# Kernel tuning notes

Hardware: AMD Instinct MI355X
Metric: run time of the kernel (lower is better)

Reference implementation:

```python
import jax, jax.numpy as jnp
import numpy as np

B, N, U = 4, 4096, 512


def setup_inputs() -> dict:
    key = jax.random.key(0)
    ks = jax.random.split(key, 5)
    s = 1.0 / np.sqrt(U)
    return {
        "x": jax.random.normal(ks[0], (B, N, U), dtype=jnp.float32),
        "Wq": jax.random.normal(ks[1], (U, U), dtype=jnp.float32) * s,
        "bq": jnp.zeros((U,), dtype=jnp.float32),
        "Wk": jax.random.normal(ks[2], (U, U), dtype=jnp.float32) * s,
        "bk": jnp.zeros((U,), dtype=jnp.float32),
        "Wv": jax.random.normal(ks[3], (U, U), dtype=jnp.float32) * s,
        "bv": jnp.zeros((U,), dtype=jnp.float32),
        "Wp": jax.random.normal(ks[4], (U, U), dtype=jnp.float32) * s,
        "bp": jnp.zeros((U,), dtype=jnp.float32),
    }


def reference(x, Wq, bq, Wk, bk, Wv, bv, Wp, bp):
    # x: [B, N, U] single-head self-attention with residual
    scale = jnp.asarray(x.shape[-1], jnp.float32) ** -0.5
    q = x @ Wq + bq
    k = x @ Wk + bk
    v = x @ Wv + bv
    scores = jnp.einsum("bnd,bmd->bnm", q, k) * scale  # [B, N, N]
    attn = jax.nn.softmax(scores, axis=-1)
    ctx = jnp.einsum("bnm,bmd->bnd", attn, v)
    return x + (ctx @ Wp + bp)
```

## Files before the change

kernel.cpp:

```cpp
#include <hip/hip_runtime.h>
#include <hip/hip_bf16.h>
#include <math.h>

#define NB 4
#define NN 4096
#define UU 512

using short8   = __attribute__((ext_vector_type(8))) short;
using bf16x8   = __attribute__((ext_vector_type(8))) __bf16;
using floatx4  = __attribute__((ext_vector_type(4))) float;
using floatx16 = __attribute__((ext_vector_type(16))) float;

__device__ __forceinline__ floatx4 mfma16(short8 a, short8 b, floatx4 c) {
    return __builtin_amdgcn_mfma_f32_16x16x32_bf16(
        __builtin_bit_cast(bf16x8, a), __builtin_bit_cast(bf16x8, b), c, 0, 0, 0);
}
__device__ __forceinline__ floatx16 mfma32(short8 a, short8 b, floatx16 c) {
    return __builtin_amdgcn_mfma_f32_32x32x16_bf16(
        __builtin_bit_cast(bf16x8, a), __builtin_bit_cast(bf16x8, b), c, 0, 0, 0);
}

__device__ __forceinline__ unsigned short f2bf(float f) {
    union { float f; unsigned u; } v; v.f = f;
    return (unsigned short)((v.u + 0x7fffu + ((v.u >> 16) & 1u)) >> 16);
}
__device__ __forceinline__ float bf2f(unsigned short s) {
    union { unsigned u; float f; } v; v.u = ((unsigned)s) << 16; return v.f;
}

#define GLL16(gp, lp) __builtin_amdgcn_global_load_lds( \
    (const __attribute__((address_space(1))) void*)(gp), \
    (__attribute__((address_space(3))) void*)(lp), 16, 0, 0)

__global__ void __launch_bounds__(256) k_cvt_x(const float* __restrict__ x,
                                               unsigned short* __restrict__ xb) {
    int i = (blockIdx.x * 256 + threadIdx.x) * 4;
    float4 v = *(const float4*)(x + i);
    ushort4 o;
    o.x = f2bf(v.x); o.y = f2bf(v.y); o.z = f2bf(v.z); o.w = f2bf(v.w);
    *(ushort4*)(xb + i) = o;
}

__global__ void __launch_bounds__(256) k_cvt_w4(
    const float* __restrict__ Wq, const float* __restrict__ Wk,
    const float* __restrict__ Wv, const float* __restrict__ Wp,
    unsigned short* __restrict__ WTbase) {
    const int z = blockIdx.y;
    const float* W = (z == 0) ? Wq : (z == 1) ? Wk : (z == 2) ? Wv : Wp;
    int idx = blockIdx.x * 256 + threadIdx.x;
    int n = idx >> 9, k = idx & 511;
    WTbase[(size_t)z * 262144 + idx] = f2bf(W[k * 512 + n]);
}

__global__ void __launch_bounds__(256, 2) k_proj(
    const unsigned short* __restrict__ Xb,
    const unsigned short* __restrict__ WqT, const unsigned short* __restrict__ WkT,
    const unsigned short* __restrict__ WvT,
    const float* __restrict__ bq, const float* __restrict__ bk, const float* __restrict__ bv,
    unsigned short* __restrict__ Q, unsigned short* __restrict__ K8,
    unsigned short* __restrict__ V8)
{
    __shared__ __align__(16) unsigned short As[128 * 32];
    __shared__ __align__(16) unsigned short Bs[128 * 32];
    const int z = blockIdx.z;
    const unsigned short* WT = (z == 0) ? WqT : (z == 1) ? WkT : WvT;
    const float* bias = (z == 0) ? bq : (z == 1) ? bk : bv;
    const int t = threadIdx.x, wave = t >> 6, lane = t & 63;
    const int quad = lane >> 4, l16 = lane & 15;
    const int m0 = blockIdx.x * 128, n0 = blockIdx.y * 128;
    const int wm = wave >> 1, wn = wave & 1;

    const int srow = wave * 32 + (lane >> 2);
    const int scol = (lane & 3) * 8;
    const unsigned short* gA = Xb + (size_t)(m0 + srow) * UU + scol;
    const unsigned short* gB = WT + (size_t)(n0 + srow) * UU + scol;
    unsigned short* lA = As + wave * 1024;
    unsigned short* lB = Bs + wave * 1024;

    floatx4 acc[4][4] = {};

    for (int k0 = 0; k0 < UU; k0 += 32) {
        GLL16(gA + k0, lA);
        GLL16(gA + k0 + 16 * UU, lA + 512);
        GLL16(gB + k0, lB);
        GLL16(gB + k0 + 16 * UU, lB + 512);
        __syncthreads();
        short8 a[4], b[4];
        #pragma unroll
        for (int i = 0; i < 4; i++)
            a[i] = *(const short8*)(As + (wm * 64 + i * 16 + l16) * 32 + quad * 8);
        #pragma unroll
        for (int j = 0; j < 4; j++)
            b[j] = *(const short8*)(Bs + (wn * 64 + j * 16 + l16) * 32 + quad * 8);
        #pragma unroll
        for (int i = 0; i < 4; i++)
            #pragma unroll
            for (int j = 0; j < 4; j++)
                acc[i][j] = mfma16(a[i], b[j], acc[i][j]);
        __syncthreads();
    }

    #pragma unroll
    for (int j = 0; j < 4; j++) {
        const int n = n0 + wn * 64 + j * 16 + l16;
        const float bv_ = bias[n];
        #pragma unroll
        for (int i = 0; i < 4; i++) {
            const int mb = m0 + wm * 64 + i * 16 + quad * 4;
            const int bb = mb >> 12, tok = mb & (NN - 1);
            if (z == 0) {
                #pragma unroll
                for (int r = 0; r < 4; r++)
                    Q[(size_t)(mb + r) * UU + n] = f2bf(acc[i][j][r] + bv_);
            } else if (z == 1) {
                const size_t base = (size_t)bb * NN * UU + (size_t)(n >> 3) * (NN * 8)
                                  + (size_t)tok * 8 + (n & 7);
                #pragma unroll
                for (int r = 0; r < 4; r++)
                    K8[base + (size_t)r * 8] = f2bf(acc[i][j][r] + bv_);
            } else {
                ushort4 o;
                o.x = f2bf(acc[i][j][0] + bv_);
                o.y = f2bf(acc[i][j][1] + bv_);
                o.z = f2bf(acc[i][j][2] + bv_);
                o.w = f2bf(acc[i][j][3] + bv_);
                *(ushort4*)(V8 + (size_t)bb * NN * UU + (size_t)(tok >> 3) * (UU * 8)
                            + (size_t)n * 8 + (tok & 7)) = o;
            }
        }
    }
}

__global__ void __launch_bounds__(512, 1) k_flash(
    const unsigned short* __restrict__ Q,
    const unsigned short* __restrict__ K8,
    const unsigned short* __restrict__ V8,
    unsigned short* __restrict__ ctx)
{
    __shared__ __align__(16) char smem[158464];
    unsigned short* Ks  = (unsigned short*)smem;
    unsigned short* Vs  = (unsigned short*)(smem + 65536);
    float*          S_f = (float*)(smem + 131072);
    unsigned short* P_l = (unsigned short*)(smem + 148480);
    float*          m_l = (float*)(smem + 157696);
    float*          l_l = m_l + 64;
    float*          a_l = m_l + 128;

    const int b = blockIdx.y, q0 = blockIdx.x * 64;
    const int t = threadIdx.x, wave = t >> 6, lane = t & 63;
    const int l31 = lane & 31, ah = lane >> 5;
    const int rg = wave >> 2, cg = (wave >> 1) & 1, dh = wave & 1;

    if (t < 64) { m_l[t] = -INFINITY; l_l[t] = 0.f; }

    const unsigned short* qp = Q + (size_t)(b * NN + q0 + rg * 32 + l31) * UU
                             + dh * 256 + ah * 8;
    short8 qf[16];
    #pragma unroll
    for (int ks = 0; ks < 16; ks++) qf[ks] = *(const short8*)(qp + ks * 16);

    const unsigned short* K8b = K8 + (size_t)b * NN * UU;
    const unsigned short* V8b = V8 + (size_t)b * NN * UU;

    #pragma unroll
    for (int j = 0; j < 8; j++) {
        const int dc = wave * 8 + j;
        GLL16(K8b + (size_t)dc * (NN * 8) + lane * 8, Ks + dc * 512 + lane * 8);
    }

    floatx16 o[4] = {};
    const float sscale = 0.04419417382415922f * 1.4426950408889634f;
    const int D0 = (cg * 2 + dh) * 128;

    __syncthreads();

    for (int kt = 0; kt < NN; kt += 64) {
        #pragma unroll
        for (int j = 0; j < 8; j++) {
            const int c = wave * 8 + j;
            GLL16(V8b + (size_t)kt * 512 + (size_t)c * 512 + lane * 8, Vs + c * 512 + lane * 8);
        }

        floatx16 sacc = {};
        #pragma unroll
        for (int ks = 0; ks < 16; ks++) {
            short8 bfrag = *(const short8*)(Ks + (dh * 32 + ks * 2 + ah) * 512
                                            + (cg * 32 + l31) * 8);
            sacc = mfma32(qf[ks], bfrag, sacc);
        }
        if (dh == 0) {
            #pragma unroll
            for (int r = 0; r < 16; r++) {
                const int row = rg * 32 + (r & 3) + 8 * (r >> 2) + 4 * ah;
                S_f[row * 68 + cg * 32 + l31] = sacc[r] * sscale;
            }
        }
        __syncthreads();
        if (dh == 1) {
            #pragma unroll
            for (int r = 0; r < 16; r++) {
                const int row = rg * 32 + (r & 3) + 8 * (r >> 2) + 4 * ah;
                S_f[row * 68 + cg * 32 + l31] += sacc[r] * sscale;
            }
        }
        __syncthreads();

        {
            const int row = t >> 3, c8 = (t & 7) * 8;
            const float4* sp = (const float4*)(S_f + row * 68 + c8);
            float4 va = sp[0], vb = sp[1];
            float mx = fmaxf(fmaxf(fmaxf(va.x, va.y), fmaxf(va.z, va.w)),
                             fmaxf(fmaxf(vb.x, vb.y), fmaxf(vb.z, vb.w)));
            mx = fmaxf(mx, __shfl_xor(mx, 1, 8));
            mx = fmaxf(mx, __shfl_xor(mx, 2, 8));
            mx = fmaxf(mx, __shfl_xor(mx, 4, 8));
            const float m_old = m_l[row];
            const float m_new = fmaxf(m_old, mx);
            float p[8] = { exp2f(va.x - m_new), exp2f(va.y - m_new),
                           exp2f(va.z - m_new), exp2f(va.w - m_new),
                           exp2f(vb.x - m_new), exp2f(vb.y - m_new),
                           exp2f(vb.z - m_new), exp2f(vb.w - m_new) };
            short8 pv; float sum = 0.f;
            #pragma unroll
            for (int j = 0; j < 8; j++) {
                unsigned short us = f2bf(p[j]);
                pv[j] = (short)us;
                sum += bf2f(us);
            }
            *(short8*)(P_l + row * 72 + c8) = pv;
            sum += __shfl_xor(sum, 1, 8);
            sum += __shfl_xor(sum, 2, 8);
            sum += __shfl_xor(sum, 4, 8);
            if ((t & 7) == 0) {
                const float alpha = exp2f(m_old - m_new);
                a_l[row] = alpha;
                m_l[row] = m_new;
                l_l[row] = l_l[row] * alpha + sum;
            }
        }
        __syncthreads();

        if (kt + 64 < NN) {
            #pragma unroll
            for (int j = 0; j < 8; j++) {
                const int dc = wave * 8 + j;
                GLL16(K8b + (size_t)dc * (NN * 8) + (size_t)(kt + 64 + lane) * 8,
                      Ks + dc * 512 + lane * 8);
            }
        }

        float alv[16];
        #pragma unroll
        for (int g = 0; g < 4; g++) {
            float4 v = *(const float4*)(a_l + rg * 32 + 4 * ah + 8 * g);
            alv[g * 4 + 0] = v.x; alv[g * 4 + 1] = v.y;
            alv[g * 4 + 2] = v.z; alv[g * 4 + 3] = v.w;
        }
        #pragma unroll
        for (int dt = 0; dt < 4; dt++)
            #pragma unroll
            for (int r = 0; r < 16; r++)
                o[dt][r] *= alv[r];

        short8 pa[4];
        #pragma unroll
        for (int ks = 0; ks < 4; ks++)
            pa[ks] = *(const short8*)(P_l + (rg * 32 + l31) * 72 + ks * 16 + ah * 8);
        #pragma unroll
        for (int dt = 0; dt < 4; dt++) {
            #pragma unroll
            for (int ks = 0; ks < 4; ks++) {
                short8 vb = *(const short8*)(Vs + (size_t)(ks * 2 + ah) * 4096
                                             + (D0 + dt * 32 + l31) * 8);
                o[dt] = mfma32(pa[ks], vb, o[dt]);
            }
        }
        __syncthreads();
    }

    float lnv[16];
    #pragma unroll
    for (int g = 0; g < 4; g++) {
        float4 v = *(const float4*)(l_l + rg * 32 + 4 * ah + 8 * g);
        lnv[g * 4 + 0] = 1.f / v.x; lnv[g * 4 + 1] = 1.f / v.y;
        lnv[g * 4 + 2] = 1.f / v.z; lnv[g * 4 + 3] = 1.f / v.w;
    }
    #pragma unroll
    for (int dt = 0; dt < 4; dt++) {
        #pragma unroll
        for (int r = 0; r < 16; r++) {
            const int row = q0 + rg * 32 + (r & 3) + 8 * (r >> 2) + 4 * ah;
            const int d = D0 + dt * 32 + l31;
            ctx[(size_t)(b * NN + row) * UU + d] = f2bf(o[dt][r] * lnv[r]);
        }
    }
}

__global__ void __launch_bounds__(256, 2) k_out(
    const unsigned short* __restrict__ Cx,
    const unsigned short* __restrict__ WpT,
    const float* __restrict__ bp,
    const float* __restrict__ x,
    float* __restrict__ out)
{
    __shared__ __align__(16) unsigned short As[128 * 32];
    __shared__ __align__(16) unsigned short Bs[128 * 32];
    const int t = threadIdx.x, wave = t >> 6, lane = t & 63;
    const int quad = lane >> 4, l16 = lane & 15;
    const int m0 = blockIdx.x * 128, n0 = blockIdx.y * 128;
    const int wm = wave >> 1, wn = wave & 1;
    const int srow = wave * 32 + (lane >> 2);
    const int scol = (lane & 3) * 8;
    const unsigned short* gA = Cx + (size_t)(m0 + srow) * UU + scol;
    const unsigned short* gB = WpT + (size_t)(n0 + srow) * UU + scol;
    unsigned short* lA = As + wave * 1024;
    unsigned short* lB = Bs + wave * 1024;

    floatx4 acc[4][4] = {};

    for (int k0 = 0; k0 < UU; k0 += 32) {
        GLL16(gA + k0, lA);
        GLL16(gA + k0 + 16 * UU, lA + 512);
        GLL16(gB + k0, lB);
        GLL16(gB + k0 + 16 * UU, lB + 512);
        __syncthreads();
        short8 a[4], b[4];
        #pragma unroll
        for (int i = 0; i < 4; i++)
            a[i] = *(const short8*)(As + (wm * 64 + i * 16 + l16) * 32 + quad * 8);
        #pragma unroll
        for (int j = 0; j < 4; j++)
            b[j] = *(const short8*)(Bs + (wn * 64 + j * 16 + l16) * 32 + quad * 8);
        #pragma unroll
        for (int i = 0; i < 4; i++)
            #pragma unroll
            for (int j = 0; j < 4; j++)
                acc[i][j] = mfma16(a[i], b[j], acc[i][j]);
        __syncthreads();
    }

    #pragma unroll
    for (int j = 0; j < 4; j++) {
        const int n = n0 + wn * 64 + j * 16 + l16;
        const float bv_ = bp[n];
        #pragma unroll
        for (int i = 0; i < 4; i++) {
            const int mb = m0 + wm * 64 + i * 16 + quad * 4;
            #pragma unroll
            for (int r = 0; r < 4; r++) {
                const size_t idx = (size_t)(mb + r) * UU + n;
                out[idx] = acc[i][j][r] + bv_ + x[idx];
            }
        }
    }
}

extern "C" void kernel_launch(void* const* d_in, const int* in_sizes, int n_in,
                              void* d_out, int out_size, void* d_ws, size_t ws_size,
                              hipStream_t stream)
{
    const float* x  = (const float*)d_in[0];
    const float* Wq = (const float*)d_in[1];
    const float* bq = (const float*)d_in[2];
    const float* Wk = (const float*)d_in[3];
    const float* bk = (const float*)d_in[4];
    const float* Wv = (const float*)d_in[5];
    const float* bv = (const float*)d_in[6];
    const float* Wp = (const float*)d_in[7];
    const float* bp = (const float*)d_in[8];
    float* out = (float*)d_out;

    char* ws = (char*)d_ws;
    unsigned short* Xb  = (unsigned short*)(ws);
    unsigned short* WTb = (unsigned short*)(ws + 16777216);
    unsigned short* WqT = WTb;
    unsigned short* WkT = WTb + 262144;
    unsigned short* WvT = WTb + 524288;
    unsigned short* WpT = WTb + 786432;
    unsigned short* Qm  = (unsigned short*)(ws + 18874368);
    unsigned short* K8m = (unsigned short*)(ws + 35651584);
    unsigned short* V8m = (unsigned short*)(ws + 52428800);
    unsigned short* Cx  = (unsigned short*)(ws + 69206016);

    hipLaunchKernelGGL(k_cvt_x, dim3(8192), dim3(256), 0, stream, x, Xb);
    hipLaunchKernelGGL(k_cvt_w4, dim3(1024, 4), dim3(256), 0, stream, Wq, Wk, Wv, Wp, WTb);
    hipLaunchKernelGGL(k_proj, dim3(128, 4, 3), dim3(256), 0, stream,
                       Xb, WqT, WkT, WvT, bq, bk, bv, Qm, K8m, V8m);
    hipLaunchKernelGGL(k_flash, dim3(64, 4), dim3(512), 0, stream, Qm, K8m, V8m, Cx);
    hipLaunchKernelGGL(k_out, dim3(128, 4), dim3(256), 0, stream, Cx, WpT, bp, x, out);
}
```

Before: 399.3 us.

## Shrink flash KV tile to 32, double-buffer V, allow two blocks per CU

The flash-attention kernel now processes 32 keys per iteration instead of 64. Each of the four waves per row group covers a 128-wide slice of the head dimension, and two score partial buffers are summed during softmax. V is double-buffered and prefetched one tile ahead. LDS use drops enough to allow two 512-thread blocks per CU. Barriers become hand-written s_waitcnt+s_barrier, and the O rescale is skipped when no row max changed. The cost is twice as many iterations, each with three to four barriers, plus register pressure from the occupancy bound of 2.

```diff
diff --git a/kernel.cpp b/kernel.cpp
--- a/kernel.cpp
+++ b/kernel.cpp
@@ -31,6 +31,9 @@
 #define GLL16(gp, lp) __builtin_amdgcn_global_load_lds( \
     (const __attribute__((address_space(1))) void*)(gp), \
     (__attribute__((address_space(3))) void*)(lp), 16, 0, 0)
+
+#define BAR_LGKM asm volatile("s_waitcnt lgkmcnt(0)\n\ts_barrier" ::: "memory")
+#define BAR_ALL  asm volatile("s_waitcnt vmcnt(0) lgkmcnt(0)\n\ts_barrier" ::: "memory")
 
 __global__ void __launch_bounds__(256) k_cvt_x(const float* __restrict__ x,
                                                unsigned short* __restrict__ xb) {
@@ -131,103 +134,111 @@
     }
 }
 
-__global__ void __launch_bounds__(512, 1) k_flash(
+__global__ void __launch_bounds__(512, 2) k_flash(
     const unsigned short* __restrict__ Q,
     const unsigned short* __restrict__ K8,
     const unsigned short* __restrict__ V8,
     unsigned short* __restrict__ ctx)
 {
-    __shared__ __align__(16) char smem[158464];
+    __shared__ __align__(16) char smem[122624];
     unsigned short* Ks  = (unsigned short*)smem;
-    unsigned short* Vs  = (unsigned short*)(smem + 65536);
-    float*          S_f = (float*)(smem + 131072);
-    unsigned short* P_l = (unsigned short*)(smem + 148480);
-    float*          m_l = (float*)(smem + 157696);
+    unsigned short* Vs0 = (unsigned short*)(smem + 32768);
+    unsigned short* Vs1 = (unsigned short*)(smem + 65536);
+    float*          Sb0 = (float*)(smem + 98304);
+    float*          Sb1 = (float*)(smem + 107520);
+    unsigned short* P_l = (unsigned short*)(smem + 116736);
+    float*          m_l = (float*)(smem + 121856);
     float*          l_l = m_l + 64;
     float*          a_l = m_l + 128;
 
     const int b = blockIdx.y, q0 = blockIdx.x * 64;
     const int t = threadIdx.x, wave = t >> 6, lane = t & 63;
     const int l31 = lane & 31, ah = lane >> 5;
-    const int rg = wave >> 2, cg = (wave >> 1) & 1, dh = wave & 1;
+    const int rg = wave >> 2, dh = wave & 3;
 
     if (t < 64) { m_l[t] = -INFINITY; l_l[t] = 0.f; }
 
     const unsigned short* qp = Q + (size_t)(b * NN + q0 + rg * 32 + l31) * UU
-                             + dh * 256 + ah * 8;
-    short8 qf[16];
-    #pragma unroll
-    for (int ks = 0; ks < 16; ks++) qf[ks] = *(const short8*)(qp + ks * 16);
+                             + dh * 128 + ah * 8;
+    short8 qf[8];
+    #pragma unroll
+    for (int ks = 0; ks < 8; ks++) qf[ks] = *(const short8*)(qp + ks * 16);
 
     const unsigned short* K8b = K8 + (size_t)b * NN * UU;
     const unsigned short* V8b = V8 + (size_t)b * NN * UU;
 
     #pragma unroll
-    for (int j = 0; j < 8; j++) {
-        const int dc = wave * 8 + j;
-        GLL16(K8b + (size_t)dc * (NN * 8) + lane * 8, Ks + dc * 512 + lane * 8);
+    for (int j = 0; j < 4; j++) {
+        const int i = wave * 4 + j;
+        GLL16(K8b + (size_t)(i * 2 + ah) * (NN * 8) + (size_t)l31 * 8,
+              Ks + i * 512 + lane * 8);
+        GLL16(V8b + (size_t)i * 512 + lane * 8, Vs0 + i * 512 + lane * 8);
     }
 
     floatx16 o[4] = {};
     const float sscale = 0.04419417382415922f * 1.4426950408889634f;
-    const int D0 = (cg * 2 + dh) * 128;
+    int cur = 0;
 
     __syncthreads();
 
-    for (int kt = 0; kt < NN; kt += 64) {
-        #pragma unroll
-        for (int j = 0; j < 8; j++) {
-            const int c = wave * 8 + j;
-            GLL16(V8b + (size_t)kt * 512 + (size_t)c * 512 + lane * 8, Vs + c * 512 + lane * 8);
+    for (int kt = 0; kt < NN; kt += 32) {
+        unsigned short* Vc = cur ? Vs1 : Vs0;
+        unsigned short* Vn = cur ? Vs0 : Vs1;
+
+        if (kt + 32 < NN) {
+            #pragma unroll
+            for (int j = 0; j < 4; j++) {
+                const int i = wave * 4 + j;
+                GLL16(V8b + (size_t)(kt + 32) * 512 + (size_t)i * 512 + lane * 8,
+                      Vn + i * 512 + lane * 8);
+            }
         }
 
         floatx16 sacc = {};
         #pragma unroll
-        for (int ks = 0; ks < 16; ks++) {
-            short8 bfrag = *(const short8*)(Ks + (dh * 32 + ks * 2 + ah) * 512
-                                            + (cg * 32 + l31) * 8);
+        for (int ks = 0; ks < 8; ks++) {
+            const int dc = dh * 16 + ks * 2 + ah;
+            short8 bfrag = *(const short8*)(Ks + dc * 256 + l31 * 8);
             sacc = mfma32(qf[ks], bfrag, sacc);
         }
-        if (dh == 0) {
+        float* Sb = (dh & 1) ? Sb1 : Sb0;
+        if (dh < 2) {
             #pragma unroll
             for (int r = 0; r < 16; r++) {
                 const int row = rg * 32 + (r & 3) + 8 * (r >> 2) + 4 * ah;
-                S_f[row * 68 + cg * 32 + l31] = sacc[r] * sscale;
-            }
-        }
-        __syncthreads();
-        if (dh == 1) {
+                Sb[row * 36 + l31] = sacc[r] * sscale;
+            }
+        }
+        BAR_LGKM;
+        if (dh >= 2) {
             #pragma unroll
             for (int r = 0; r < 16; r++) {
                 const int row = rg * 32 + (r & 3) + 8 * (r >> 2) + 4 * ah;
-                S_f[row * 68 + cg * 32 + l31] += sacc[r] * sscale;
-            }
-        }
-        __syncthreads();
+                Sb[row * 36 + l31] += sacc[r] * sscale;
+            }
+        }
+        BAR_LGKM;
 
         {
-            const int row = t >> 3, c8 = (t & 7) * 8;
-            const float4* sp = (const float4*)(S_f + row * 68 + c8);
-            float4 va = sp[0], vb = sp[1];
-            float mx = fmaxf(fmaxf(fmaxf(va.x, va.y), fmaxf(va.z, va.w)),
-                             fmaxf(fmaxf(vb.x, vb.y), fmaxf(vb.z, vb.w)));
+            const int row = t >> 3, c4 = (t & 7) * 4;
+            float4 v0 = *(const float4*)(Sb0 + row * 36 + c4);
+            float4 v1 = *(const float4*)(Sb1 + row * 36 + c4);
+            float4 s;
+            s.x = v0.x + v1.x; s.y = v0.y + v1.y;
+            s.z = v0.z + v1.z; s.w = v0.w + v1.w;
+            float mx = fmaxf(fmaxf(s.x, s.y), fmaxf(s.z, s.w));
             mx = fmaxf(mx, __shfl_xor(mx, 1, 8));
             mx = fmaxf(mx, __shfl_xor(mx, 2, 8));
             mx = fmaxf(mx, __shfl_xor(mx, 4, 8));
             const float m_old = m_l[row];
             const float m_new = fmaxf(m_old, mx);
-            float p[8] = { exp2f(va.x - m_new), exp2f(va.y - m_new),
-                           exp2f(va.z - m_new), exp2f(va.w - m_new),
-                           exp2f(vb.x - m_new), exp2f(vb.y - m_new),
-                           exp2f(vb.z - m_new), exp2f(vb.w - m_new) };
-            short8 pv; float sum = 0.f;
-            #pragma unroll
-            for (int j = 0; j < 8; j++) {
-                unsigned short us = f2bf(p[j]);
-                pv[j] = (short)us;
-                sum += bf2f(us);
-            }
-            *(short8*)(P_l + row * 72 + c8) = pv;
+            ushort4 pv;
+            pv.x = f2bf(exp2f(s.x - m_new));
+            pv.y = f2bf(exp2f(s.y - m_new));
+            pv.z = f2bf(exp2f(s.z - m_new));
+            pv.w = f2bf(exp2f(s.w - m_new));
+            float sum = bf2f(pv.x) + bf2f(pv.y) + bf2f(pv.z) + bf2f(pv.w);
+            *(ushort4*)(P_l + row * 40 + c4) = pv;
             sum += __shfl_xor(sum, 1, 8);
             sum += __shfl_xor(sum, 2, 8);
             sum += __shfl_xor(sum, 4, 8);
@@ -238,50 +249,55 @@
                 l_l[row] = l_l[row] * alpha + sum;
             }
         }
-        __syncthreads();
-
-        if (kt + 64 < NN) {
-            #pragma unroll
-            for (int j = 0; j < 8; j++) {
-                const int dc = wave * 8 + j;
-                GLL16(K8b + (size_t)dc * (NN * 8) + (size_t)(kt + 64 + lane) * 8,
-                      Ks + dc * 512 + lane * 8);
+        BAR_LGKM;
+
+        if (kt + 32 < NN) {
+            #pragma unroll
+            for (int j = 0; j < 4; j++) {
+                const int i = wave * 4 + j;
+                GLL16(K8b + (size_t)(i * 2 + ah) * (NN * 8) + (size_t)(kt + 32 + l31) * 8,
+                      Ks + i * 512 + lane * 8);
             }
         }
 
         float alv[16];
         #pragma unroll
         for (int g = 0; g < 4; g++) {
-            float4 v = *(const float4*)(a_l + rg * 32 + 4 * ah + 8 * g);
+            float4 v = *(const float4*)(a_l + rg * 32 + ah * 4 + g * 8);
             alv[g * 4 + 0] = v.x; alv[g * 4 + 1] = v.y;
             alv[g * 4 + 2] = v.z; alv[g * 4 + 3] = v.w;
         }
-        #pragma unroll
-        for (int dt = 0; dt < 4; dt++)
-            #pragma unroll
-            for (int r = 0; r < 16; r++)
-                o[dt][r] *= alv[r];
-
-        short8 pa[4];
-        #pragma unroll
-        for (int ks = 0; ks < 4; ks++)
-            pa[ks] = *(const short8*)(P_l + (rg * 32 + l31) * 72 + ks * 16 + ah * 8);
+        bool ns = false;
+        #pragma unroll
+        for (int r = 0; r < 16; r++) ns |= (alv[r] != 1.0f);
+        if (__any(ns)) {
+            #pragma unroll
+            for (int dt = 0; dt < 4; dt++)
+                #pragma unroll
+                for (int r = 0; r < 16; r++)
+                    o[dt][r] *= alv[r];
+        }
+        short8 pa[2];
+        #pragma unroll
+        for (int ks = 0; ks < 2; ks++)
+            pa[ks] = *(const short8*)(P_l + (rg * 32 + l31) * 40 + ks * 16 + ah * 8);
         #pragma unroll
         for (int dt = 0; dt < 4; dt++) {
             #pragma unroll
-            for (int ks = 0; ks < 4; ks++) {
-                short8 vb = *(const short8*)(Vs + (size_t)(ks * 2 + ah) * 4096
-                                             + (D0 + dt * 32 + l31) * 8);
+            for (int ks = 0; ks < 2; ks++) {
+                short8 vb = *(const short8*)(Vc + (ks * 2 + ah) * 4096
+                                             + (dh * 128 + dt * 32 + l31) * 8);
                 o[dt] = mfma32(pa[ks], vb, o[dt]);
             }
         }
-        __syncthreads();
+        BAR_ALL;
+        cur ^= 1;
     }
 
     float lnv[16];
     #pragma unroll
     for (int g = 0; g < 4; g++) {
-        float4 v = *(const float4*)(l_l + rg * 32 + 4 * ah + 8 * g);
+        float4 v = *(const float4*)(l_l + rg * 32 + ah * 4 + g * 8);
         lnv[g * 4 + 0] = 1.f / v.x; lnv[g * 4 + 1] = 1.f / v.y;
         lnv[g * 4 + 2] = 1.f / v.z; lnv[g * 4 + 3] = 1.f / v.w;
     }
@@ -290,7 +306,7 @@
         #pragma unroll
         for (int r = 0; r < 16; r++) {
             const int row = q0 + rg * 32 + (r & 3) + 8 * (r >> 2) + 4 * ah;
-            const int d = D0 + dt * 32 + l31;
+            const int d = dh * 128 + dt * 32 + l31;
             ctx[(size_t)(b * NN + row) * UU + d] = f2bf(o[dt][r] * lnv[r]);
         }
     }
```

Measured after the change: 498.1 us. 1.25x slower.

## Restructure flash kernel into 32-row blocks with split-D partial scores and direct global loads

Applied to the files above, without the earlier changes.

The flash kernel now processes 32 query rows per block instead of 64, with each of 8 waves owning a 64-wide slice of the head dimension. Each wave computes partial QK^T scores that are reduced through shared memory. K and V fragments are read straight from global memory into registers instead of being staged through large LDS tiles. This cuts LDS use so up to 4 blocks can be resident per CU and doubles the grid, and it skips rescaling the output when the running max does not change. In exchange, K/V traffic from global/L2 doubles because each block covers fewer query rows, and the loop now issues a block-wide reduction with two barriers every 32 keys.

```diff
diff --git a/kernel.cpp b/kernel.cpp
--- a/kernel.cpp
+++ b/kernel.cpp
@@ -131,166 +131,174 @@
     }
 }
 
-__global__ void __launch_bounds__(512, 1) k_flash(
+__global__ void __launch_bounds__(512, 4) k_flash(
     const unsigned short* __restrict__ Q,
     const unsigned short* __restrict__ K8,
     const unsigned short* __restrict__ V8,
     unsigned short* __restrict__ ctx)
 {
-    __shared__ __align__(16) char smem[158464];
-    unsigned short* Ks  = (unsigned short*)smem;
-    unsigned short* Vs  = (unsigned short*)(smem + 65536);
-    float*          S_f = (float*)(smem + 131072);
-    unsigned short* P_l = (unsigned short*)(smem + 148480);
-    float*          m_l = (float*)(smem + 157696);
-    float*          l_l = m_l + 64;
-    float*          a_l = m_l + 128;
-
-    const int b = blockIdx.y, q0 = blockIdx.x * 64;
-    const int t = threadIdx.x, wave = t >> 6, lane = t & 63;
+    __shared__ __align__(16) float Sb[8][32 * 33];
+    __shared__ __align__(16) unsigned short P_l[32 * 36];
+    __shared__ float m_l[32], l_l[32], a_l[32];
+
+    const int b = blockIdx.y, q0 = blockIdx.x * 32;
+    const int t = threadIdx.x, w = t >> 6, lane = t & 63;
     const int l31 = lane & 31, ah = lane >> 5;
-    const int rg = wave >> 2, cg = (wave >> 1) & 1, dh = wave & 1;
-
-    if (t < 64) { m_l[t] = -INFINITY; l_l[t] = 0.f; }
-
-    const unsigned short* qp = Q + (size_t)(b * NN + q0 + rg * 32 + l31) * UU
-                             + dh * 256 + ah * 8;
-    short8 qf[16];
-    #pragma unroll
-    for (int ks = 0; ks < 16; ks++) qf[ks] = *(const short8*)(qp + ks * 16);
+
+    if (t < 32) { m_l[t] = -INFINITY; l_l[t] = 0.f; }
+
+    const unsigned short* qp = Q + (size_t)(b * NN + q0 + l31) * UU + w * 64 + ah * 8;
+    short8 qf[4];
+    #pragma unroll
+    for (int ks = 0; ks < 4; ks++) qf[ks] = *(const short8*)(qp + ks * 16);
 
     const unsigned short* K8b = K8 + (size_t)b * NN * UU;
     const unsigned short* V8b = V8 + (size_t)b * NN * UU;
-
-    #pragma unroll
-    for (int j = 0; j < 8; j++) {
-        const int dc = wave * 8 + j;
-        GLL16(K8b + (size_t)dc * (NN * 8) + lane * 8, Ks + dc * 512 + lane * 8);
-    }
-
-    floatx16 o[4] = {};
     const float sscale = 0.04419417382415922f * 1.4426950408889634f;
-    const int D0 = (cg * 2 + dh) * 128;
-
+
+    {
+        floatx16 sacc = {};
+        #pragma unroll
+        for (int ks = 0; ks < 4; ks++) {
+            short8 kf = *(const short8*)(K8b + (size_t)(w * 8 + ks * 2 + ah) * (NN * 8)
+                                         + (size_t)l31 * 8);
+            sacc = mfma32(qf[ks], kf, sacc);
+        }
+        #pragma unroll
+        for (int r = 0; r < 16; r++)
+            Sb[w][((r & 3) + 8 * (r >> 2) + 4 * ah) * 33 + l31] = sacc[r] * sscale;
+    }
     __syncthreads();
-
-    for (int kt = 0; kt < NN; kt += 64) {
-        #pragma unroll
-        for (int j = 0; j < 8; j++) {
-            const int c = wave * 8 + j;
-            GLL16(V8b + (size_t)kt * 512 + (size_t)c * 512 + lane * 8, Vs + c * 512 + lane * 8);
-        }
-
-        floatx16 sacc = {};
-        #pragma unroll
-        for (int ks = 0; ks < 16; ks++) {
-            short8 bfrag = *(const short8*)(Ks + (dh * 32 + ks * 2 + ah) * 512
-                                            + (cg * 32 + l31) * 8);
-            sacc = mfma32(qf[ks], bfrag, sacc);
-        }
-        if (dh == 0) {
-            #pragma unroll
-            for (int r = 0; r < 16; r++) {
-                const int row = rg * 32 + (r & 3) + 8 * (r >> 2) + 4 * ah;
-                S_f[row * 68 + cg * 32 + l31] = sacc[r] * sscale;
-            }
-        }
-        __syncthreads();
-        if (dh == 1) {
-            #pragma unroll
-            for (int r = 0; r < 16; r++) {
-                const int row = rg * 32 + (r & 3) + 8 * (r >> 2) + 4 * ah;
-                S_f[row * 68 + cg * 32 + l31] += sacc[r] * sscale;
-            }
-        }
-        __syncthreads();
-
-        {
-            const int row = t >> 3, c8 = (t & 7) * 8;
-            const float4* sp = (const float4*)(S_f + row * 68 + c8);
-            float4 va = sp[0], vb = sp[1];
-            float mx = fmaxf(fmaxf(fmaxf(va.x, va.y), fmaxf(va.z, va.w)),
-                             fmaxf(fmaxf(vb.x, vb.y), fmaxf(vb.z, vb.w)));
-            mx = fmaxf(mx, __shfl_xor(mx, 1, 8));
-            mx = fmaxf(mx, __shfl_xor(mx, 2, 8));
-            mx = fmaxf(mx, __shfl_xor(mx, 4, 8));
-            const float m_old = m_l[row];
-            const float m_new = fmaxf(m_old, mx);
-            float p[8] = { exp2f(va.x - m_new), exp2f(va.y - m_new),
-                           exp2f(va.z - m_new), exp2f(va.w - m_new),
-                           exp2f(vb.x - m_new), exp2f(vb.y - m_new),
-                           exp2f(vb.z - m_new), exp2f(vb.w - m_new) };
-            short8 pv; float sum = 0.f;
-            #pragma unroll
-            for (int j = 0; j < 8; j++) {
-                unsigned short us = f2bf(p[j]);
-                pv[j] = (short)us;
-                sum += bf2f(us);
-            }
-            *(short8*)(P_l + row * 72 + c8) = pv;
-            sum += __shfl_xor(sum, 1, 8);
-            sum += __shfl_xor(sum, 2, 8);
-            sum += __shfl_xor(sum, 4, 8);
-            if ((t & 7) == 0) {
-                const float alpha = exp2f(m_old - m_new);
-                a_l[row] = alpha;
-                m_l[row] = m_new;
-                l_l[row] = l_l[row] * alpha + sum;
-            }
-        }
-        __syncthreads();
-
-        if (kt + 64 < NN) {
-            #pragma unroll
-            for (int j = 0; j < 8; j++) {
-                const int dc = wave * 8 + j;
-                GLL16(K8b + (size_t)dc * (NN * 8) + (size_t)(kt + 64 + lane) * 8,
-                      Ks + dc * 512 + lane * 8);
-            }
-        }
-
+    {
+        const int row = t >> 4, c0 = (t & 15) * 2;
+        float s0 = 0.f, s1 = 0.f;
+        #pragma unroll
+        for (int u = 0; u < 8; u++) {
+            float2 v = *(const float2*)(&Sb[u][row * 33 + c0]);
+            s0 += v.x; s1 += v.y;
+        }
+        float mx = fmaxf(s0, s1);
+        mx = fmaxf(mx, __shfl_xor(mx, 1, 16));
+        mx = fmaxf(mx, __shfl_xor(mx, 2, 16));
+        mx = fmaxf(mx, __shfl_xor(mx, 4, 16));
+        mx = fmaxf(mx, __shfl_xor(mx, 8, 16));
+        const float m_old = m_l[row];
+        const float m_new = fmaxf(m_old, mx);
+        ushort2 pv;
+        pv.x = f2bf(exp2f(s0 - m_new));
+        pv.y = f2bf(exp2f(s1 - m_new));
+        *(ushort2*)(P_l + row * 36 + c0) = pv;
+        float sum = bf2f(pv.x) + bf2f(pv.y);
+        sum += __shfl_xor(sum, 1, 16);
+        sum += __shfl_xor(sum, 2, 16);
+        sum += __shfl_xor(sum, 4, 16);
+        sum += __shfl_xor(sum, 8, 16);
+        if ((t & 15) == 0) {
+            const float alpha = exp2f(m_old - m_new);
+            a_l[row] = alpha;
+            m_l[row] = m_new;
+            l_l[row] = l_l[row] * alpha + sum;
+        }
+    }
+    __syncthreads();
+
+    floatx16 o[2] = {};
+
+    for (int kt = 0; kt < NN; kt += 32) {
+        short8 vf[2][2];
+        #pragma unroll
+        for (int ks = 0; ks < 2; ks++)
+            #pragma unroll
+            for (int dt = 0; dt < 2; dt++)
+                vf[ks][dt] = *(const short8*)(V8b + (size_t)((kt >> 3) + ks * 2 + ah) * (UU * 8)
+                                              + (size_t)(w * 64 + dt * 32 + l31) * 8);
         float alv[16];
         #pragma unroll
         for (int g = 0; g < 4; g++) {
-            float4 v = *(const float4*)(a_l + rg * 32 + 4 * ah + 8 * g);
+            float4 v = *(const float4*)(a_l + ah * 4 + g * 8);
             alv[g * 4 + 0] = v.x; alv[g * 4 + 1] = v.y;
             alv[g * 4 + 2] = v.z; alv[g * 4 + 3] = v.w;
         }
-        #pragma unroll
-        for (int dt = 0; dt < 4; dt++)
+        bool ns = false;
+        #pragma unroll
+        for (int r = 0; r < 16; r++) ns |= (alv[r] != 1.0f);
+        if (__any(ns)) {
+            #pragma unroll
+            for (int dt = 0; dt < 2; dt++)
+                #pragma unroll
+                for (int r = 0; r < 16; r++)
+                    o[dt][r] *= alv[r];
+        }
+        short8 pa[2];
+        #pragma unroll
+        for (int ks = 0; ks < 2; ks++)
+            pa[ks] = *(const short8*)(P_l + l31 * 36 + ks * 16 + ah * 8);
+        #pragma unroll
+        for (int dt = 0; dt < 2; dt++)
+            #pragma unroll
+            for (int ks = 0; ks < 2; ks++)
+                o[dt] = mfma32(pa[ks], vf[ks][dt], o[dt]);
+
+        if (kt + 32 < NN) {
+            floatx16 sacc = {};
+            #pragma unroll
+            for (int ks = 0; ks < 4; ks++) {
+                short8 kf = *(const short8*)(K8b + (size_t)(w * 8 + ks * 2 + ah) * (NN * 8)
+                                             + (size_t)(kt + 32 + l31) * 8);
+                sacc = mfma32(qf[ks], kf, sacc);
+            }
             #pragma unroll
             for (int r = 0; r < 16; r++)
-                o[dt][r] *= alv[r];
-
-        short8 pa[4];
-        #pragma unroll
-        for (int ks = 0; ks < 4; ks++)
-            pa[ks] = *(const short8*)(P_l + (rg * 32 + l31) * 72 + ks * 16 + ah * 8);
-        #pragma unroll
-        for (int dt = 0; dt < 4; dt++) {
-            #pragma unroll
-            for (int ks = 0; ks < 4; ks++) {
-                short8 vb = *(const short8*)(Vs + (size_t)(ks * 2 + ah) * 4096
-                                             + (D0 + dt * 32 + l31) * 8);
-                o[dt] = mfma32(pa[ks], vb, o[dt]);
+                Sb[w][((r & 3) + 8 * (r >> 2) + 4 * ah) * 33 + l31] = sacc[r] * sscale;
+            __syncthreads();
+            {
+                const int row = t >> 4, c0 = (t & 15) * 2;
+                float s0 = 0.f, s1 = 0.f;
+                #pragma unroll
+                for (int u = 0; u < 8; u++) {
+                    float2 v = *(const float2*)(&Sb[u][row * 33 + c0]);
+                    s0 += v.x; s1 += v.y;
+                }
+                float mx = fmaxf(s0, s1);
+                mx = fmaxf(mx, __shfl_xor(mx, 1, 16));
+                mx = fmaxf(mx, __shfl_xor(mx, 2, 16));
+                mx = fmaxf(mx, __shfl_xor(mx, 4, 16));
+                mx = fmaxf(mx, __shfl_xor(mx, 8, 16));
+                const float m_old = m_l[row];
+                const float m_new = fmaxf(m_old, mx);
+                ushort2 pv;
+                pv.x = f2bf(exp2f(s0 - m_new));
+                pv.y = f2bf(exp2f(s1 - m_new));
+                *(ushort2*)(P_l + row * 36 + c0) = pv;
+                float sum = bf2f(pv.x) + bf2f(pv.y);
+                sum += __shfl_xor(sum, 1, 16);
+                sum += __shfl_xor(sum, 2, 16);
+                sum += __shfl_xor(sum, 4, 16);
+                sum += __shfl_xor(sum, 8, 16);
+                if ((t & 15) == 0) {
+                    const float alpha = exp2f(m_old - m_new);
+                    a_l[row] = alpha;
+                    m_l[row] = m_new;
+                    l_l[row] = l_l[row] * alpha + sum;
+                }
             }
-        }
-        __syncthreads();
+            __syncthreads();
+        }
     }
 
     float lnv[16];
     #pragma unroll
     for (int g = 0; g < 4; g++) {
-        float4 v = *(const float4*)(l_l + rg * 32 + 4 * ah + 8 * g);
+        float4 v = *(const float4*)(l_l + ah * 4 + g * 8);
         lnv[g * 4 + 0] = 1.f / v.x; lnv[g * 4 + 1] = 1.f / v.y;
         lnv[g * 4 + 2] = 1.f / v.z; lnv[g * 4 + 3] = 1.f / v.w;
     }
     #pragma unroll
-    for (int dt = 0; dt < 4; dt++) {
+    for (int dt = 0; dt < 2; dt++) {
         #pragma unroll
         for (int r = 0; r < 16; r++) {
-            const int row = q0 + rg * 32 + (r & 3) + 8 * (r >> 2) + 4 * ah;
-            const int d = D0 + dt * 32 + l31;
+            const int row = q0 + (r & 3) + 8 * (r >> 2) + 4 * ah;
+            const int d = w * 64 + dt * 32 + l31;
             ctx[(size_t)(b * NN + row) * UU + d] = f2bf(o[dt][r] * lnv[r]);
         }
     }
@@ -386,6 +394,6 @@
     hipLaunchKernelGGL(k_cvt_w4, dim3(1024, 4), dim3(256), 0, stream, Wq, Wk, Wv, Wp, WTb);
     hipLaunchKernelGGL(k_proj, dim3(128, 4, 3), dim3(256), 0, stream,
                        Xb, WqT, WkT, WvT, bq, bk, bv, Qm, K8m, V8m);
-    hipLaunchKernelGGL(k_flash, dim3(64, 4), dim3(512), 0, stream, Qm, K8m, V8m, Cx);
+    hipLaunchKernelGGL(k_flash, dim3(128, 4), dim3(512), 0, stream, Qm, K8m, V8m, Cx);
     hipLaunchKernelGGL(k_out, dim3(128, 4), dim3(256), 0, stream, Cx, WpT, bp, x, out);
 }
```

New measurement: 455.8 us. 1.14x slower.
